# Kernel tuning notes

Measured on AMD Instinct MI355X. Metric: run time of the kernel, lower is better.

## Reference

```python
import jax, jax.numpy as jnp
import numpy as np

D = 512        # model dim
NH = 8         # heads
NL = 4         # layers
MSL = 2048     # max_seq_len for relative positional bias
ITEM_V, CATE_V, SEG_V = 100000, 1000, 2
EPS = 1e-5


def layer_norm(x, w, b):
    mu = jnp.mean(x, axis=-1, keepdims=True)
    var = jnp.mean((x - mu) ** 2, axis=-1, keepdims=True)
    return (x - mu) * jax.lax.rsqrt(var + EPS) * w + b


def setup_inputs() -> dict:
    key = jax.random.key(0)
    ks = jax.random.split(key, 16)
    B, L = 8, 1023
    inp = {
        'historical_item_ids': jax.random.randint(ks[0], (B, L), 0, ITEM_V, dtype=jnp.int32),
        'historical_cate_ids': jax.random.randint(ks[1], (B, L), 0, CATE_V, dtype=jnp.int32),
        'historical_len': jax.random.randint(ks[2], (B,), 0, L, dtype=jnp.int32),
        'target_item_id': jax.random.randint(ks[3], (B,), 0, ITEM_V, dtype=jnp.int32),
        'target_cate_id': jax.random.randint(ks[4], (B,), 0, CATE_V, dtype=jnp.int32),
        # embeddings (init std 0.02 like _init_weights)
        'item_emb': 0.02 * jax.random.normal(ks[5], (ITEM_V, D), jnp.float32),
        'cate_emb': 0.02 * jax.random.normal(ks[6], (CATE_V, D), jnp.float32),
        'seg_emb': 0.02 * jax.random.normal(ks[7], (SEG_V, D), jnp.float32),
        # per-layer stacked params
        'W1': 0.02 * jax.random.normal(ks[8], (NL, D, 4 * D), jnp.float32),
        'b1': jnp.zeros((NL, 4 * D), jnp.float32),
        'W2': 0.02 * jax.random.normal(ks[9], (NL, D, D), jnp.float32),
        'b2': jnp.zeros((NL, D), jnp.float32),
        'ln1_w': jnp.ones((NL, D), jnp.float32), 'ln1_b': jnp.zeros((NL, D), jnp.float32),
        'ln2_w': jnp.ones((NL, D), jnp.float32), 'ln2_b': jnp.zeros((NL, D), jnp.float32),
        'pos_w': 0.02 * jax.random.normal(ks[10], (NL, 2 * MSL - 1), jnp.float32),
        'lnf_w': jnp.ones((D,), jnp.float32), 'lnf_b': jnp.zeros((D,), jnp.float32),
    }
    return inp


def _forward(historical_item_ids, historical_cate_ids, historical_len,
             target_item_id, target_cate_id,
             item_emb, cate_emb, seg_emb, W1, b1, W2, b2,
             ln1_w, ln1_b, ln2_w, ln2_b, pos_w, lnf_w, lnf_b):
    B = historical_item_ids.shape[0]
    ar = jnp.arange(B)
    pad = jnp.zeros((B, 1), historical_item_ids.dtype)
    ids = jnp.concatenate([historical_item_ids, pad], axis=1).at[ar, historical_len].set(target_item_id)
    cids = jnp.concatenate([historical_cate_ids, pad], axis=1).at[ar, historical_len].set(target_cate_id)
    S = ids.shape[1]
    seg = jnp.zeros_like(ids).at[ar, historical_len].set(1)

    h = item_emb[ids] + cate_emb[cids] + seg_emb[seg]  # [B,S,D]

    # relative position bias indices: bias[i,j] = pos_w[MSL-1 + j - i]
    rel_idx = MSL - 1 + jnp.arange(S)[None, :] - jnp.arange(S)[:, None]  # [S,S]
    causal = jnp.tril(jnp.ones((S, S), h.dtype))  # multiplicative mask (mask >= 0)

    for l in range(NL):
        z = jax.nn.silu(h @ W1[l] + b1[l])  # [B,S,4D]
        u, q, k, v = jnp.split(z, 4, axis=-1)
        resh = lambda t: t.reshape(B, S, NH, D // NH).transpose(0, 2, 1, 3)  # [B,H,S,hd]
        u, q, k, v = resh(u), resh(q), resh(k), resh(v)
        bias = pos_w[l][rel_idx]  # [S,S]
        att = jax.nn.silu(jnp.einsum('bhsd,bhtd->bhst', q, k) + bias) * causal
        y = jnp.einsum('bhst,bhtd->bhsd', att, v) * u
        y = y.transpose(0, 2, 1, 3).reshape(B, S, D)
        y = layer_norm(y, ln1_w[l], ln1_b[l])
        y = y @ W2[l] + b2[l]
        h = layer_norm(y + h, ln2_w[l], ln2_b[l])  # dropout p=0 (eval)

    return layer_norm(h, lnf_w, lnf_b)


def reference(historical_item_ids, historical_cate_ids, historical_len,
              target_item_id, target_cate_id,
              item_emb, cate_emb, seg_emb, W1, b1, W2, b2,
              ln1_w, ln1_b, ln2_w, ln2_b, pos_w, lnf_w, lnf_b):
    return _forward(historical_item_ids, historical_cate_ids, historical_len,
                    target_item_id, target_cate_id,
                    item_emb, cate_emb, seg_emb, W1, b1, W2, b2,
                    ln1_w, ln1_b, ln2_w, ln2_b, pos_w, lnf_w, lnf_b)
```

## Files before the change

### kernel.cpp

```cpp
#include <hip/hip_runtime.h>
#include <cstddef>


#define D_MODEL 512
#define S_LEN 1024
#define NHEADS 8

typedef __bf16 bf16x8 __attribute__((ext_vector_type(8)));
typedef float f32x4 __attribute__((ext_vector_type(4)));
typedef unsigned short us4 __attribute__((ext_vector_type(4)));
typedef unsigned short us8 __attribute__((ext_vector_type(8)));

__device__ __forceinline__ float silu_f(float x) {
  return x / (1.f + __expf(-x));
}
__device__ __forceinline__ unsigned short f2bf(float f) {
  unsigned int u = __float_as_uint(f);
  u += 0x7FFF + ((u >> 16) & 1);
  return (unsigned short)(u >> 16);
}
__device__ __forceinline__ float bf2f(unsigned short s) {
  return __uint_as_float(((unsigned int)s) << 16);
}
__device__ __forceinline__ void gll16(const void* g, void* l) {
  __builtin_amdgcn_global_load_lds(
      (const __attribute__((address_space(1))) unsigned int*)g,
      (__attribute__((address_space(3))) unsigned int*)l, 16, 0, 0);
}

__global__ __launch_bounds__(256) void embed_kernel(
    const int* __restrict__ hist_i, const int* __restrict__ hist_c,
    const int* __restrict__ hlen, const int* __restrict__ tgt_i,
    const int* __restrict__ tgt_c, const float* __restrict__ item_emb,
    const float* __restrict__ cate_emb, const float* __restrict__ seg_emb,
    float* __restrict__ h32, unsigned short* __restrict__ hbf) {
  int bs = blockIdx.x;
  int b = bs >> 10, s = bs & 1023;
  int l = hlen[b];
  int id, cid, sg;
  if (s == l)       { id = tgt_i[b]; cid = tgt_c[b]; sg = 1; }
  else if (s < 1023){ id = hist_i[b * 1023 + s]; cid = hist_c[b * 1023 + s]; sg = 0; }
  else              { id = 0; cid = 0; sg = 0; }
  const float* ie = item_emb + (size_t)id * D_MODEL;
  const float* ce = cate_emb + (size_t)cid * D_MODEL;
  const float* se = seg_emb + (size_t)sg * D_MODEL;
  float* hr = h32 + (size_t)bs * D_MODEL;
  unsigned short* hb = hbf + (size_t)bs * D_MODEL;
  for (int d = threadIdx.x; d < D_MODEL; d += 256) {
    float v = ie[d] + ce[d] + se[d];
    hr[d] = v;
    hb[d] = f2bf(v);
  }
}

__global__ __launch_bounds__(256) void transpose_kernel(
    const float* __restrict__ W, unsigned short* __restrict__ Wt,
    int K, int N) {
  const int l = blockIdx.z;
  W += (size_t)l * K * N;
  Wt += (size_t)l * K * N;
  const int n0 = blockIdx.x * 64, k0 = blockIdx.y * 64;
  __shared__ float T[64][65];
  const int tid = threadIdx.x;
  const int rr = tid >> 4, cc = (tid & 15) * 4;
#pragma unroll
  for (int p = 0; p < 4; p++) {
    const int r = rr + p * 16;
    const float4 v = *reinterpret_cast<const float4*>(&W[(size_t)(k0 + r) * N + n0 + cc]);
    T[r][cc] = v.x; T[r][cc + 1] = v.y; T[r][cc + 2] = v.z; T[r][cc + 3] = v.w;
  }
  __syncthreads();
#pragma unroll
  for (int p = 0; p < 4; p++) {
    const int r = rr + p * 16;
    us4 o = { f2bf(T[cc + 0][r]), f2bf(T[cc + 1][r]),
              f2bf(T[cc + 2][r]), f2bf(T[cc + 3][r]) };
    *reinterpret_cast<us4*>(&Wt[(size_t)(n0 + r) * K + k0 + cc]) = o;
  }
}

template <int TM, int TN, int WR, int WC, int SWZ, int EPI_SILU, typename OutT>
__global__ __launch_bounds__(WR * WC * 64) void mfma_gemm(
    const unsigned short* __restrict__ A, const unsigned short* __restrict__ Bt,
    const float* __restrict__ bias, OutT* __restrict__ C,
    int M, int N, int K) {
  constexpr int NT = WR * WC * 64;
  constexpr int WM = TM / WR, WN = TN / WC;
  constexpr int MI = WM / 16, NI = WN / 16;
  __shared__ unsigned short As[2][TM * 64];
  __shared__ unsigned short Bs[2][TN * 64];
  const int tid = threadIdx.x;
  const int w = tid >> 6, lane = tid & 63, lm = lane & 15, quad = lane >> 4;
  const int wm = w % WR, wn = w / WR;
  int m0, n0;
  if (SWZ) {
    const int id = blockIdx.x;
    const int xcd = id & 7, j = id >> 3;
    const int mPerX = (M / TM) >> 3;
    m0 = (xcd * mPerX + (j % mPerX)) * TM;
    n0 = (j / mPerX) * TN;
  } else {
    m0 = blockIdx.y * TM;
    n0 = blockIdx.x * TN;
  }

  f32x4 acc[MI][NI] = {};

  auto stage = [&](int buf, int k0) {
#pragma unroll
    for (int p = 0; p < TM * 8 / NT; p++) {
      const int g = p * NT + tid;
      const int r = g >> 3;
      const int lc = (g & 7) ^ (r & 7);
      gll16(A + (size_t)(m0 + r) * K + k0 + lc * 8, &As[buf][g * 8]);
    }
#pragma unroll
    for (int p = 0; p < TN * 8 / NT; p++) {
      const int g = p * NT + tid;
      const int r = g >> 3;
      const int lc = (g & 7) ^ (r & 7);
      gll16(Bt + (size_t)(n0 + r) * K + k0 + lc * 8, &Bs[buf][g * 8]);
    }
  };

  stage(0, 0);
  __syncthreads();
  int cur = 0;

  for (int k0 = 0; k0 < K; k0 += 64) {
    if (k0 + 64 < K) stage(cur ^ 1, k0 + 64);
#pragma unroll
    for (int ki = 0; ki < 2; ki++) {
      bf16x8 af[MI], bfr[NI];
#pragma unroll
      for (int mi = 0; mi < MI; mi++) {
        const int r = wm * WM + mi * 16 + lm;
        const int p = (ki * 4 + quad) ^ (lm & 7);
        af[mi] = *reinterpret_cast<const bf16x8*>(&As[cur][r * 64 + p * 8]);
      }
#pragma unroll
      for (int ni = 0; ni < NI; ni++) {
        const int r = wn * WN + ni * 16 + lm;
        const int p = (ki * 4 + quad) ^ (lm & 7);
        bfr[ni] = *reinterpret_cast<const bf16x8*>(&Bs[cur][r * 64 + p * 8]);
      }
#pragma unroll
      for (int mi = 0; mi < MI; mi++)
#pragma unroll
        for (int ni = 0; ni < NI; ni++)
          acc[mi][ni] = __builtin_amdgcn_mfma_f32_16x16x32_bf16(
              af[mi], bfr[ni], acc[mi][ni], 0, 0, 0);
    }
    __syncthreads();
    cur ^= 1;
  }

#pragma unroll
  for (int ni = 0; ni < NI; ni++) {
    const int n = n0 + wn * WN + ni * 16 + lm;
    const float bv = bias[n];
#pragma unroll
    for (int mi = 0; mi < MI; mi++) {
      const int mbase = m0 + wm * WM + mi * 16 + quad * 4;
#pragma unroll
      for (int reg = 0; reg < 4; reg++) {
        float v = acc[mi][ni][reg] + bv;
        if (EPI_SILU) v = silu_f(v);
        if constexpr (sizeof(OutT) == 2)
          C[(size_t)(mbase + reg) * N + n] = f2bf(v);
        else
          C[(size_t)(mbase + reg) * N + n] = v;
      }
    }
  }
}

#define LDR 72
__global__ __launch_bounds__(256) void attn_kernel(
    const unsigned short* __restrict__ z, const float* __restrict__ posw,
    unsigned short* __restrict__ y) {
  const int hh = blockIdx.y, b = blockIdx.z;
  __shared__ alignas(16) unsigned short Ks[2 * 64 * LDR];
  __shared__ alignas(16) unsigned short Vt[2 * 64 * LDR];
  __shared__ alignas(16) unsigned short Ps[64 * LDR];
  __shared__ float bias_s[2][128];
  const unsigned short* zb = z + (size_t)b * S_LEN * 2048;
  const int tid = threadIdx.x;
  const int w = tid >> 6, lane = tid & 63, lm = lane & 15, quad = lane >> 4;

  const int kr0r = tid >> 3, kr0c = (tid & 7) * 8;
  const int kr1r = (256 + tid) >> 3, kr1c = (tid & 7) * 8;
  const int vt = (tid >> 4) * 4, vd = (tid & 15) * 4;
  const int vtb = vt >> 3, vti = vt & 7;

#pragma unroll
  for (int phase = 0; phase < 2; phase++) {
    const int qt = phase == 0 ? (int)blockIdx.x : 15 - (int)blockIdx.x;
    const int s0 = qt * 64;
    const int srow = s0 + w * 16 + lm;

    const bf16x8 qb0 = *reinterpret_cast<const bf16x8*>(
        zb + (size_t)srow * 2048 + 512 + hh * 64 + quad * 8);
    const bf16x8 qb1 = *reinterpret_cast<const bf16x8*>(
        zb + (size_t)srow * 2048 + 512 + hh * 64 + 32 + quad * 8);

    f32x4 O[4] = {};

    us8 kr0, kr1;
    us4 vr0, vr1, vr2, vr3;
    float br = 0.f;

    auto load_stage = [&](int kt) {
      const int t0 = kt * 64;
      kr0 = *reinterpret_cast<const us8*>(
          zb + (size_t)(t0 + kr0r) * 2048 + 1024 + hh * 64 + kr0c);
      kr1 = *reinterpret_cast<const us8*>(
          zb + (size_t)(t0 + kr1r) * 2048 + 1024 + hh * 64 + kr1c);
      vr0 = *reinterpret_cast<const us4*>(
          zb + (size_t)(t0 + vt + 0) * 2048 + 1536 + hh * 64 + vd);
      vr1 = *reinterpret_cast<const us4*>(
          zb + (size_t)(t0 + vt + 1) * 2048 + 1536 + hh * 64 + vd);
      vr2 = *reinterpret_cast<const us4*>(
          zb + (size_t)(t0 + vt + 2) * 2048 + 1536 + hh * 64 + vd);
      vr3 = *reinterpret_cast<const us4*>(
          zb + (size_t)(t0 + vt + 3) * 2048 + 1536 + hh * 64 + vd);
      if (tid < 128) br = posw[2047 + t0 - s0 - 63 + tid];
    };

    auto write_stage = [&](int cur) {
      unsigned short* KsC = Ks + cur * (64 * LDR);
      unsigned short* VtC = Vt + cur * (64 * LDR);
      *reinterpret_cast<us8*>(&KsC[kr0r * LDR + kr0c]) = kr0;
      *reinterpret_cast<us8*>(&KsC[kr1r * LDR + kr1c]) = kr1;
      unsigned short c[4][4];
      c[0][0] = vr0.x; c[0][1] = vr0.y; c[0][2] = vr0.z; c[0][3] = vr0.w;
      c[1][0] = vr1.x; c[1][1] = vr1.y; c[1][2] = vr1.z; c[1][3] = vr1.w;
      c[2][0] = vr2.x; c[2][1] = vr2.y; c[2][2] = vr2.z; c[2][3] = vr2.w;
      c[3][0] = vr3.x; c[3][1] = vr3.y; c[3][2] = vr3.z; c[3][3] = vr3.w;
#pragma unroll
      for (int j = 0; j < 4; j++) {
        const int dd = vd + j;
        us4 o = { c[0][j], c[1][j], c[2][j], c[3][j] };
        *reinterpret_cast<us4*>(&VtC[dd * LDR + ((vtb ^ (dd & 7)) << 3) + vti]) = o;
      }
      if (tid < 128) bias_s[cur][tid] = br;
    };

    load_stage(0);
    __syncthreads();

    for (int kt = 0; kt <= qt; kt++) {
      const int cur = kt & 1;
      write_stage(cur);
      __syncthreads();
      if (kt < qt) load_stage(kt + 1);

      const unsigned short* KsC = Ks + cur * (64 * LDR);
      const unsigned short* VtC = Vt + cur * (64 * LDR);
      const int t0 = kt * 64;

#pragma unroll
      for (int tt = 0; tt < 4; tt++) {
        const bf16x8 ka0 = *reinterpret_cast<const bf16x8*>(
            &KsC[(tt * 16 + lm) * LDR + quad * 8]);
        const bf16x8 ka1 = *reinterpret_cast<const bf16x8*>(
            &KsC[(tt * 16 + lm) * LDR + 32 + quad * 8]);
        f32x4 st = {};
        __builtin_amdgcn_s_setprio(1);
        st = __builtin_amdgcn_mfma_f32_16x16x32_bf16(ka0, qb0, st, 0, 0, 0);
        st = __builtin_amdgcn_mfma_f32_16x16x32_bf16(ka1, qb1, st, 0, 0, 0);
        __builtin_amdgcn_s_setprio(0);
        const int bbase = 63 + tt * 16 + quad * 4 - w * 16 - lm;
        const int tq = t0 + tt * 16 + quad * 4;
        us4 pv;
        unsigned short* pp = (unsigned short*)&pv;
#pragma unroll
        for (int i = 0; i < 4; i++) {
          const float x = st[i] + bias_s[cur][bbase + i];
          const float val = (tq + i <= srow) ? silu_f(x) : 0.f;
          pp[i] = f2bf(val);
        }
        *reinterpret_cast<us4*>(&Ps[(w * 16 + lm) * LDR + tt * 16 + quad * 4]) = pv;
      }

      const bf16x8 pa0 = *reinterpret_cast<const bf16x8*>(
          &Ps[(w * 16 + lm) * LDR + quad * 8]);
      const bf16x8 pa1 = *reinterpret_cast<const bf16x8*>(
          &Ps[(w * 16 + lm) * LDR + 32 + quad * 8]);
#pragma unroll
      for (int ct = 0; ct < 4; ct++) {
        const int d = ct * 16 + lm;
        const bf16x8 vb0 = *reinterpret_cast<const bf16x8*>(
            &VtC[d * LDR + ((quad ^ (d & 7)) << 3)]);
        const bf16x8 vb1 = *reinterpret_cast<const bf16x8*>(
            &VtC[d * LDR + (((4 + quad) ^ (d & 7)) << 3)]);
        __builtin_amdgcn_s_setprio(1);
        O[ct] = __builtin_amdgcn_mfma_f32_16x16x32_bf16(pa0, vb0, O[ct], 0, 0, 0);
        O[ct] = __builtin_amdgcn_mfma_f32_16x16x32_bf16(pa1, vb1, O[ct], 0, 0, 0);
        __builtin_amdgcn_s_setprio(0);
      }
    }

    {
      const int sbase = s0 + w * 16 + quad * 4;
#pragma unroll
      for (int ct = 0; ct < 4; ct++) {
        const int d = ct * 16 + lm;
#pragma unroll
        for (int i = 0; i < 4; i++) {
          const int sg = sbase + i;
          const float u = bf2f(zb[(size_t)sg * 2048 + hh * 64 + d]);
          y[((size_t)(b * S_LEN + sg)) * D_MODEL + hh * 64 + d] = f2bf(O[ct][i] * u);
        }
      }
    }
  }
}

template <typename XT>
__global__ __launch_bounds__(256) void ln_kernel(
    const XT* __restrict__ x, const float* __restrict__ res,
    const float* __restrict__ w, const float* __restrict__ bb,
    float* __restrict__ o32, unsigned short* __restrict__ obf) {
  const int wv = threadIdx.x >> 6, lane = threadIdx.x & 63;
  const size_t row = blockIdx.x * 4 + wv;
  const int c0 = lane * 8;
  float v[8];
  if constexpr (sizeof(XT) == 2) {
    const us8 u = *reinterpret_cast<const us8*>(&x[row * D_MODEL + c0]);
#pragma unroll
    for (int i = 0; i < 8; i++) v[i] = bf2f(u[i]);
  } else {
    const float4 a = *reinterpret_cast<const float4*>(&x[row * D_MODEL + c0]);
    const float4 c = *reinterpret_cast<const float4*>(&x[row * D_MODEL + c0 + 4]);
    v[0] = a.x; v[1] = a.y; v[2] = a.z; v[3] = a.w;
    v[4] = c.x; v[5] = c.y; v[6] = c.z; v[7] = c.w;
  }
  if (res) {
    const float4 r0 = *reinterpret_cast<const float4*>(&res[row * D_MODEL + c0]);
    const float4 r1 = *reinterpret_cast<const float4*>(&res[row * D_MODEL + c0 + 4]);
    v[0] += r0.x; v[1] += r0.y; v[2] += r0.z; v[3] += r0.w;
    v[4] += r1.x; v[5] += r1.y; v[6] += r1.z; v[7] += r1.w;
  }
  float s = 0.f, ss = 0.f;
#pragma unroll
  for (int i = 0; i < 8; i++) { s += v[i]; ss += v[i] * v[i]; }
#pragma unroll
  for (int off = 32; off; off >>= 1) {
    s += __shfl_down(s, off, 64);
    ss += __shfl_down(ss, off, 64);
  }
  s = __shfl(s, 0, 64);
  ss = __shfl(ss, 0, 64);
  const float mu = s * (1.f / D_MODEL);
  const float rstd = rsqrtf(ss * (1.f / D_MODEL) - mu * mu + 1e-5f);
  const float4 w0 = *reinterpret_cast<const float4*>(&w[c0]);
  const float4 w1 = *reinterpret_cast<const float4*>(&w[c0 + 4]);
  const float4 b0 = *reinterpret_cast<const float4*>(&bb[c0]);
  const float4 b1 = *reinterpret_cast<const float4*>(&bb[c0 + 4]);
  float r[8];
  r[0] = (v[0] - mu) * rstd * w0.x + b0.x;
  r[1] = (v[1] - mu) * rstd * w0.y + b0.y;
  r[2] = (v[2] - mu) * rstd * w0.z + b0.z;
  r[3] = (v[3] - mu) * rstd * w0.w + b0.w;
  r[4] = (v[4] - mu) * rstd * w1.x + b1.x;
  r[5] = (v[5] - mu) * rstd * w1.y + b1.y;
  r[6] = (v[6] - mu) * rstd * w1.z + b1.z;
  r[7] = (v[7] - mu) * rstd * w1.w + b1.w;
  if (o32) {
    *reinterpret_cast<float4*>(&o32[row * D_MODEL + c0]) = make_float4(r[0], r[1], r[2], r[3]);
    *reinterpret_cast<float4*>(&o32[row * D_MODEL + c0 + 4]) = make_float4(r[4], r[5], r[6], r[7]);
  }
  if (obf) {
    us8 q = { f2bf(r[0]), f2bf(r[1]), f2bf(r[2]), f2bf(r[3]),
              f2bf(r[4]), f2bf(r[5]), f2bf(r[6]), f2bf(r[7]) };
    *reinterpret_cast<us8*>(&obf[row * D_MODEL + c0]) = q;
  }
}

extern "C" void kernel_launch(void* const* d_in, const int* in_sizes, int n_in,
                              void* d_out, int out_size, void* d_ws, size_t ws_size,
                              hipStream_t stream) {
  const int* hist_i = (const int*)d_in[0];
  const int* hist_c = (const int*)d_in[1];
  const int* hlen   = (const int*)d_in[2];
  const int* tgt_i  = (const int*)d_in[3];
  const int* tgt_c  = (const int*)d_in[4];
  const float* item_emb = (const float*)d_in[5];
  const float* cate_emb = (const float*)d_in[6];
  const float* seg_emb  = (const float*)d_in[7];
  const float* W1   = (const float*)d_in[8];
  const float* b1   = (const float*)d_in[9];
  const float* W2   = (const float*)d_in[10];
  const float* b2   = (const float*)d_in[11];
  const float* ln1w = (const float*)d_in[12];
  const float* ln1b = (const float*)d_in[13];
  const float* ln2w = (const float*)d_in[14];
  const float* ln2b = (const float*)d_in[15];
  const float* posw = (const float*)d_in[16];
  const float* lnfw = (const float*)d_in[17];
  const float* lnfb = (const float*)d_in[18];
  float* out = (float*)d_out;

  char* ws = (char*)d_ws;
  float*          h32 = (float*)(ws);
  unsigned short* hbf = (unsigned short*)(ws + (16u << 20));
  unsigned short* zbf = (unsigned short*)(ws + (24u << 20));
  unsigned short* ybf = (unsigned short*)(ws + (56u << 20));
  unsigned short* yab = (unsigned short*)(ws + (64u << 20));
  unsigned short* tbf = yab;
  unsigned short* W1t = (unsigned short*)(ws + (80u << 20));
  unsigned short* W2t = (unsigned short*)(ws + (88u << 20));

  const int ROWS = 8 * S_LEN;

  transpose_kernel<<<dim3(2048 / 64, 512 / 64, 4), 256, 0, stream>>>(W1, W1t, 512, 2048);
  transpose_kernel<<<dim3(512 / 64, 512 / 64, 4), 256, 0, stream>>>(W2, W2t, 512, 512);
  embed_kernel<<<ROWS, 256, 0, stream>>>(hist_i, hist_c, hlen, tgt_i, tgt_c,
                                         item_emb, cate_emb, seg_emb, h32, hbf);
  for (int l = 0; l < 4; l++) {
    mfma_gemm<128, 128, 2, 4, 1, 1, unsigned short><<<1024, 512, 0, stream>>>(
        hbf, W1t + (size_t)l * 2048 * 512, b1 + (size_t)l * 2048, zbf, ROWS, 2048, 512);
    attn_kernel<<<dim3(8, NHEADS, 8), 256, 0, stream>>>(
        zbf, posw + (size_t)l * 4095, yab);
    ln_kernel<unsigned short><<<ROWS / 4, 256, 0, stream>>>(
        yab, nullptr, ln1w + l * 512, ln1b + l * 512, nullptr, ybf);
    mfma_gemm<64, 128, 2, 2, 0, 0, unsigned short><<<dim3(512 / 128, ROWS / 64), 256, 0, stream>>>(
        ybf, W2t + (size_t)l * 512 * 512, b2 + (size_t)l * 512, tbf, ROWS, 512, 512);
    ln_kernel<unsigned short><<<ROWS / 4, 256, 0, stream>>>(
        tbf, h32, ln2w + l * 512, ln2b + l * 512, h32, hbf);
  }
  ln_kernel<float><<<ROWS / 4, 256, 0, stream>>>(h32, nullptr, lnfw, lnfb, out, nullptr);
}
```

Measured before the change: 744.4 us.

## Fold LN1 into second GEMM via precomputed weight scaling and row statistics

Removes the separate LN1 kernel by folding ln1 weight into the transposed W2 and precomputing c1=ln1w·W2 and c2=ln1b·W2 per layer. The new GEMM computes row mean and sum of squares on the fly from the A tiles and applies LN algebraically in the epilogue. This saves one full read/write pass over the activation per layer. In exchange it uses the one-pass E[x²]-μ² variance, which is less stable, and it applies bf16 rounding to scaled weights.

```diff
diff --git a/kernel.cpp b/kernel.cpp
--- a/kernel.cpp
+++ b/kernel.cpp
@@ -55,10 +55,11 @@
 
 __global__ __launch_bounds__(256) void transpose_kernel(
     const float* __restrict__ W, unsigned short* __restrict__ Wt,
-    int K, int N) {
+    int K, int N, const float* __restrict__ lnw) {
   const int l = blockIdx.z;
   W += (size_t)l * K * N;
   Wt += (size_t)l * K * N;
+  if (lnw) lnw += (size_t)l * K;
   const int n0 = blockIdx.x * 64, k0 = blockIdx.y * 64;
   __shared__ float T[64][65];
   const int tid = threadIdx.x;
@@ -70,12 +71,42 @@
     T[r][cc] = v.x; T[r][cc + 1] = v.y; T[r][cc + 2] = v.z; T[r][cc + 3] = v.w;
   }
   __syncthreads();
+  float l0 = 1.f, l1 = 1.f, l2 = 1.f, l3 = 1.f;
+  if (lnw) { l0 = lnw[k0 + cc]; l1 = lnw[k0 + cc + 1];
+             l2 = lnw[k0 + cc + 2]; l3 = lnw[k0 + cc + 3]; }
 #pragma unroll
   for (int p = 0; p < 4; p++) {
     const int r = rr + p * 16;
-    us4 o = { f2bf(T[cc + 0][r]), f2bf(T[cc + 1][r]),
-              f2bf(T[cc + 2][r]), f2bf(T[cc + 3][r]) };
+    us4 o = { f2bf(T[cc + 0][r] * l0), f2bf(T[cc + 1][r] * l1),
+              f2bf(T[cc + 2][r] * l2), f2bf(T[cc + 3][r] * l3) };
     *reinterpret_cast<us4*>(&Wt[(size_t)(n0 + r) * K + k0 + cc]) = o;
+  }
+}
+
+__global__ __launch_bounds__(256) void c12_kernel(
+    const float* __restrict__ W2, const float* __restrict__ ln1w,
+    const float* __restrict__ ln1b, float* __restrict__ c1,
+    float* __restrict__ c2) {
+  const int l = blockIdx.y;
+  const int nl = threadIdx.x & 63;
+  const int n = blockIdx.x * 64 + nl;
+  const int kp = threadIdx.x >> 6;
+  const float* W = W2 + (size_t)l * 512 * 512;
+  const float* lw = ln1w + (size_t)l * 512;
+  const float* lb = ln1b + (size_t)l * 512;
+  float s1 = 0.f, s2 = 0.f;
+  for (int k = kp * 128; k < kp * 128 + 128; k++) {
+    const float wv = W[(size_t)k * 512 + n];
+    s1 += lw[k] * wv;
+    s2 += lb[k] * wv;
+  }
+  __shared__ float r1[4][64], r2[4][64];
+  r1[kp][nl] = s1;
+  r2[kp][nl] = s2;
+  __syncthreads();
+  if (kp == 0) {
+    c1[(size_t)l * 512 + n] = r1[0][nl] + r1[1][nl] + r1[2][nl] + r1[3][nl];
+    c2[(size_t)l * 512 + n] = r2[0][nl] + r2[1][nl] + r2[2][nl] + r2[3][nl];
   }
 }
 
@@ -175,6 +206,129 @@
   }
 }
 
+__global__ __launch_bounds__(256) void gemm2_ln1(
+    const unsigned short* __restrict__ A, const unsigned short* __restrict__ Bt,
+    const float* __restrict__ b2, const float* __restrict__ c1,
+    const float* __restrict__ c2, unsigned short* __restrict__ C) {
+  constexpr int TM = 64, TN = 128, NT = 256, K = 512, N = 512;
+  constexpr int MI = 2, NI = 4;
+  __shared__ unsigned short As[2][TM * 64];
+  __shared__ unsigned short Bs[2][TN * 64];
+  __shared__ float rsum[64], rssum[64];
+  const int tid = threadIdx.x;
+  const int w = tid >> 6, lane = tid & 63, lm = lane & 15, quad = lane >> 4;
+  const int wm = w & 1, wn = w >> 1;
+  const int m0 = blockIdx.y * TM, n0 = blockIdx.x * TN;
+
+  f32x4 acc[MI][NI] = {};
+  float sA[MI] = {0.f, 0.f}, ssA[MI] = {0.f, 0.f};
+
+  auto stage = [&](int buf, int k0) {
+#pragma unroll
+    for (int p = 0; p < 2; p++) {
+      const int g = p * NT + tid;
+      const int r = g >> 3;
+      const int lc = (g & 7) ^ (r & 7);
+      gll16(A + (size_t)(m0 + r) * K + k0 + lc * 8, &As[buf][g * 8]);
+    }
+#pragma unroll
+    for (int p = 0; p < 4; p++) {
+      const int g = p * NT + tid;
+      const int r = g >> 3;
+      const int lc = (g & 7) ^ (r & 7);
+      gll16(Bt + (size_t)(n0 + r) * K + k0 + lc * 8, &Bs[buf][g * 8]);
+    }
+  };
+
+  stage(0, 0);
+  __syncthreads();
+  int cur = 0;
+  for (int k0 = 0; k0 < K; k0 += 64) {
+    if (k0 + 64 < K) stage(cur ^ 1, k0 + 64);
+#pragma unroll
+    for (int ki = 0; ki < 2; ki++) {
+      bf16x8 af[MI], bfr[NI];
+#pragma unroll
+      for (int mi = 0; mi < MI; mi++) {
+        const int r = wm * 32 + mi * 16 + lm;
+        const int p = (ki * 4 + quad) ^ (lm & 7);
+        af[mi] = *reinterpret_cast<const bf16x8*>(&As[cur][r * 64 + p * 8]);
+      }
+#pragma unroll
+      for (int ni = 0; ni < NI; ni++) {
+        const int r = wn * 64 + ni * 16 + lm;
+        const int p = (ki * 4 + quad) ^ (lm & 7);
+        bfr[ni] = *reinterpret_cast<const bf16x8*>(&Bs[cur][r * 64 + p * 8]);
+      }
+      if (wn == 0) {
+#pragma unroll
+        for (int mi = 0; mi < MI; mi++) {
+          const us8 u = *reinterpret_cast<const us8*>(&af[mi]);
+#pragma unroll
+          for (int e = 0; e < 8; e++) {
+            const float x = bf2f(u[e]);
+            sA[mi] += x;
+            ssA[mi] += x * x;
+          }
+        }
+      }
+#pragma unroll
+      for (int mi = 0; mi < MI; mi++)
+#pragma unroll
+        for (int ni = 0; ni < NI; ni++)
+          acc[mi][ni] = __builtin_amdgcn_mfma_f32_16x16x32_bf16(
+              af[mi], bfr[ni], acc[mi][ni], 0, 0, 0);
+    }
+    __syncthreads();
+    cur ^= 1;
+  }
+
+  if (wn == 0) {
+#pragma unroll
+    for (int mi = 0; mi < MI; mi++) {
+      float s = sA[mi], ss = ssA[mi];
+      s += __shfl_xor(s, 16, 64);
+      s += __shfl_xor(s, 32, 64);
+      ss += __shfl_xor(ss, 16, 64);
+      ss += __shfl_xor(ss, 32, 64);
+      if (quad == 0) {
+        rsum[wm * 32 + mi * 16 + lm] = s;
+        rssum[wm * 32 + mi * 16 + lm] = ss;
+      }
+    }
+  }
+  __syncthreads();
+
+  float rs8[MI][4], rm8[MI][4];
+#pragma unroll
+  for (int mi = 0; mi < MI; mi++)
+#pragma unroll
+    for (int reg = 0; reg < 4; reg++) {
+      const int lr = wm * 32 + mi * 16 + quad * 4 + reg;
+      const float mu = rsum[lr] * (1.f / 512.f);
+      const float var = rssum[lr] * (1.f / 512.f) - mu * mu;
+      const float rs = rsqrtf(var + 1e-5f);
+      rs8[mi][reg] = rs;
+      rm8[mi][reg] = rs * mu;
+    }
+
+#pragma unroll
+  for (int ni = 0; ni < NI; ni++) {
+    const int n = n0 + wn * 64 + ni * 16 + lm;
+    const float c1v = c1[n];
+    const float bv = c2[n] + b2[n];
+#pragma unroll
+    for (int mi = 0; mi < MI; mi++) {
+      const int mbase = m0 + wm * 32 + mi * 16 + quad * 4;
+#pragma unroll
+      for (int reg = 0; reg < 4; reg++) {
+        const float v = rs8[mi][reg] * acc[mi][ni][reg] - rm8[mi][reg] * c1v + bv;
+        C[(size_t)(mbase + reg) * N + n] = f2bf(v);
+      }
+    }
+  }
+}
+
 #define LDR 72
 __global__ __launch_bounds__(256) void attn_kernel(
     const unsigned short* __restrict__ z, const float* __restrict__ posw,
@@ -406,16 +560,20 @@
   float*          h32 = (float*)(ws);
   unsigned short* hbf = (unsigned short*)(ws + (16u << 20));
   unsigned short* zbf = (unsigned short*)(ws + (24u << 20));
-  unsigned short* ybf = (unsigned short*)(ws + (56u << 20));
+  unsigned short* tbf = (unsigned short*)(ws + (56u << 20));
   unsigned short* yab = (unsigned short*)(ws + (64u << 20));
-  unsigned short* tbf = yab;
+  float*          c1g = (float*)(ws + (72u << 20));
+  float*          c2g = (float*)(ws + (72u << 20) + 8192);
   unsigned short* W1t = (unsigned short*)(ws + (80u << 20));
   unsigned short* W2t = (unsigned short*)(ws + (88u << 20));
 
   const int ROWS = 8 * S_LEN;
 
-  transpose_kernel<<<dim3(2048 / 64, 512 / 64, 4), 256, 0, stream>>>(W1, W1t, 512, 2048);
-  transpose_kernel<<<dim3(512 / 64, 512 / 64, 4), 256, 0, stream>>>(W2, W2t, 512, 512);
+  transpose_kernel<<<dim3(2048 / 64, 512 / 64, 4), 256, 0, stream>>>(
+      W1, W1t, 512, 2048, nullptr);
+  transpose_kernel<<<dim3(512 / 64, 512 / 64, 4), 256, 0, stream>>>(
+      W2, W2t, 512, 512, ln1w);
+  c12_kernel<<<dim3(8, 4), 256, 0, stream>>>(W2, ln1w, ln1b, c1g, c2g);
   embed_kernel<<<ROWS, 256, 0, stream>>>(hist_i, hist_c, hlen, tgt_i, tgt_c,
                                          item_emb, cate_emb, seg_emb, h32, hbf);
   for (int l = 0; l < 4; l++) {
@@ -423,10 +581,9 @@
         hbf, W1t + (size_t)l * 2048 * 512, b1 + (size_t)l * 2048, zbf, ROWS, 2048, 512);
     attn_kernel<<<dim3(8, NHEADS, 8), 256, 0, stream>>>(
         zbf, posw + (size_t)l * 4095, yab);
-    ln_kernel<unsigned short><<<ROWS / 4, 256, 0, stream>>>(
-        yab, nullptr, ln1w + l * 512, ln1b + l * 512, nullptr, ybf);
-    mfma_gemm<64, 128, 2, 2, 0, 0, unsigned short><<<dim3(512 / 128, ROWS / 64), 256, 0, stream>>>(
-        ybf, W2t + (size_t)l * 512 * 512, b2 + (size_t)l * 512, tbf, ROWS, 512, 512);
+    gemm2_ln1<<<dim3(512 / 128, ROWS / 64), 256, 0, stream>>>(
+        yab, W2t + (size_t)l * 512 * 512, b2 + (size_t)l * 512,
+        c1g + (size_t)l * 512, c2g + (size_t)l * 512, tbf);
     ln_kernel<unsigned short><<<ROWS / 4, 256, 0, stream>>>(
         tbf, h32, ln2w + l * 512, ln2b + l * 512, h32, hbf);
   }
```

New measurement: 735.3 us. About the same (-1.2%).
